# Kernel tuning notes

Hardware: AMD Instinct MI355X
Metric: run time of the kernel (lower is better)

## Reference

```python
import jax, jax.numpy as jnp
import numpy as np

B, S, D = 2, 2048, 1024
H = 16
HD = D // H  # 64
SCALE = HD ** -0.5


def setup_inputs() -> dict:
    key = jax.random.key(0)
    ks = jax.random.split(key, 9)
    init = lambda k, shape: jax.random.normal(k, shape, dtype=jnp.float32) * (1.0 / np.sqrt(shape[-1]))
    return {
        "x": jax.random.normal(ks[0], (B, S, D), dtype=jnp.float32),
        "wq": init(ks[1], (D, D)), "bq": jnp.zeros((D,), jnp.float32),
        "wk": init(ks[2], (D, D)), "bk": jnp.zeros((D,), jnp.float32),
        "wv": init(ks[3], (D, D)), "bv": jnp.zeros((D,), jnp.float32),
        "wo": init(ks[4], (D, D)), "bo": jnp.zeros((D,), jnp.float32),
    }


def reference(x, wq, bq, wk, bk, wv, bv, wo, bo):
    b, s, d = x.shape
    # projections -> [b, h, s, hd]
    q = (x @ wq + bq).reshape(b, s, H, HD).transpose(0, 2, 1, 3)
    k = (x @ wk + bk).reshape(b, s, H, HD).transpose(0, 2, 1, 3)
    v = (x @ wv + bv).reshape(b, s, H, HD).transpose(0, 2, 1, 3)
    # full causal attention (chunked loop in original computes exactly this)
    scores = jnp.einsum("bhqd,bhkd->bhqk", q, k) * SCALE
    causal = jnp.tril(jnp.ones((s, s), dtype=bool))
    scores = jnp.where(causal, scores, -jnp.inf)
    weights = jax.nn.softmax(scores, axis=-1)
    out = jnp.einsum("bhqk,bhkd->bhqd", weights, v)
    out = out.transpose(0, 2, 1, 3).reshape(b, s, d)
    return out @ wo + bo
```

## Files before the change

kernel.cpp:

```cpp
#include <hip/hip_runtime.h>
#include <hip/hip_bf16.h>
#include <cstdint>

#define B_  2
#define S_  2048
#define D_  1024
#define H_  16
#define HD_ 64
#define M_  (B_ * S_)
static constexpr float SC_LOG2E = 0.125f * 1.44269504088896f;

typedef __bf16 bf16x8 __attribute__((ext_vector_type(8)));
typedef __bf16 bf16x4 __attribute__((ext_vector_type(4)));
typedef float  f32x4  __attribute__((ext_vector_type(4)));

__device__ __forceinline__ unsigned short f2b(float f) {
  union { float f; unsigned u; } x; x.f = f;
  unsigned r = x.u + 0x7FFF + ((x.u >> 16) & 1);
  return (unsigned short)(r >> 16);
}

__device__ __forceinline__ void gl_lds16(const unsigned short* g, unsigned short* l) {
  __builtin_amdgcn_global_load_lds((const __attribute__((address_space(1))) void*)g,
                                   (__attribute__((address_space(3))) void*)l, 16, 0, 0);
}

__global__ void cvt_all_kernel(const float* __restrict__ x,
                               const float* __restrict__ w0, const float* __restrict__ w1,
                               const float* __restrict__ w2, const float* __restrict__ w3,
                               unsigned short* __restrict__ xb,
                               unsigned short* __restrict__ o0, unsigned short* __restrict__ o1,
                               unsigned short* __restrict__ o2, unsigned short* __restrict__ o3) {
  int tx = threadIdx.x, ty = threadIdx.y;
  if (blockIdx.z == 4) {
    int tid = ty * 32 + tx;
    int base = ((int)blockIdx.y * 32 + (int)blockIdx.x) * 1024 + tid;
    const float4* xf = (const float4*)x;
    ushort4* ob = (ushort4*)xb;
#pragma unroll
    for (int j = 0; j < 4; j++) {
      float4 v = xf[base + j * 256];
      ushort4 r;
      r.x = f2b(v.x); r.y = f2b(v.y); r.z = f2b(v.z); r.w = f2b(v.w);
      ob[base + j * 256] = r;
    }
    return;
  }
  const float* w = blockIdx.z == 0 ? w0 : blockIdx.z == 1 ? w1 : blockIdx.z == 2 ? w2 : w3;
  unsigned short* o = blockIdx.z == 0 ? o0 : blockIdx.z == 1 ? o1 : blockIdx.z == 2 ? o2 : o3;
  __shared__ float t[32][33];
  int x0 = blockIdx.x * 32, y0 = blockIdx.y * 32;
#pragma unroll
  for (int j = 0; j < 4; j++)
    t[ty + j * 8][tx] = w[(size_t)(y0 + ty + j * 8) * D_ + x0 + tx];
  __syncthreads();
#pragma unroll
  for (int j = 0; j < 4; j++)
    o[(size_t)(x0 + ty + j * 8) * D_ + y0 + tx] = f2b(t[tx][ty + j * 8]);
}

__global__ __launch_bounds__(256) void qkv_gemm_kernel(
    const unsigned short* __restrict__ xb,
    const unsigned short* __restrict__ wqt, const unsigned short* __restrict__ wkt,
    const unsigned short* __restrict__ wvt,
    const float* __restrict__ bq, const float* __restrict__ bk, const float* __restrict__ bv,
    unsigned short* __restrict__ qo, unsigned short* __restrict__ ko, unsigned short* __restrict__ vo) {
  const unsigned short* wt = blockIdx.z == 0 ? wqt : blockIdx.z == 1 ? wkt : wvt;
  const float* bias        = blockIdx.z == 0 ? bq  : blockIdx.z == 1 ? bk  : bv;
  unsigned short* out      = blockIdx.z == 0 ? qo  : blockIdx.z == 1 ? ko  : vo;
  const float scl = blockIdx.z == 0 ? SC_LOG2E : 1.0f;

  __shared__ __align__(16) unsigned short smem[4 * 128 * 32];
  unsigned short* pan[4] = { smem, smem + 4096, smem + 8192, smem + 12288 };
  const int tid = threadIdx.x;
  const int lane = tid & 63, wid = tid >> 6;
  const int wm = wid & 1, wn = wid >> 1;
  const int m0 = blockIdx.x * 128, n0 = blockIdx.y * 128;
  const int l15 = lane & 15, q4 = lane >> 4;

  f32x4 zero = {0.f, 0.f, 0.f, 0.f};
  f32x4 acc[4][4];
#pragma unroll
  for (int mt = 0; mt < 4; mt++)
#pragma unroll
    for (int nt = 0; nt < 4; nt++) acc[mt][nt] = zero;

  for (int kk = 0; kk < D_; kk += 64) {
#pragma unroll
    for (int i = 0; i < 2; i++) {
      int ci = tid + i * 256;
      int row = ci >> 2, kc = ci & 3;
      gl_lds16(xb + (size_t)(m0 + row) * D_ + kk      + kc * 8, pan[0] + ci * 8);
      gl_lds16(xb + (size_t)(m0 + row) * D_ + kk + 32 + kc * 8, pan[1] + ci * 8);
      gl_lds16(wt + (size_t)(n0 + row) * D_ + kk      + kc * 8, pan[2] + ci * 8);
      gl_lds16(wt + (size_t)(n0 + row) * D_ + kk + 32 + kc * 8, pan[3] + ci * 8);
    }
    __syncthreads();
#pragma unroll
    for (int kh = 0; kh < 2; kh++) {
      bf16x8 af[4], bfv[4];
#pragma unroll
      for (int mt = 0; mt < 4; mt++) af[mt]  = *(const bf16x8*)(pan[kh]     + (wm * 64 + mt * 16 + l15) * 32 + q4 * 8);
#pragma unroll
      for (int nt = 0; nt < 4; nt++) bfv[nt] = *(const bf16x8*)(pan[2 + kh] + (wn * 64 + nt * 16 + l15) * 32 + q4 * 8);
#pragma unroll
      for (int mt = 0; mt < 4; mt++)
#pragma unroll
        for (int nt = 0; nt < 4; nt++)
          acc[mt][nt] = __builtin_amdgcn_mfma_f32_16x16x32_bf16(af[mt], bfv[nt], acc[mt][nt], 0, 0, 0);
    }
    __syncthreads();
  }

  if (blockIdx.z < 2) {
#pragma unroll
    for (int nt = 0; nt < 4; nt++) {
      int n = n0 + wn * 64 + nt * 16 + l15;
      float bn = bias[n];
      int h = n >> 6, hd = n & 63;
#pragma unroll
      for (int mt = 0; mt < 4; mt++) {
#pragma unroll
        for (int r = 0; r < 4; r++) {
          int m = m0 + wm * 64 + mt * 16 + q4 * 4 + r;
          int b = m >> 11, s = m & (S_ - 1);
          out[(((size_t)(b * H_ + h)) * S_ + s) * HD_ + hd] = f2b((acc[mt][nt][r] + bn) * scl);
        }
      }
    }
  } else {
    unsigned short* buf = smem;
#pragma unroll
    for (int p = 0; p < 2; p++) {
      __syncthreads();
      if (wn == p) {
#pragma unroll
        for (int nt = 0; nt < 4; nt++) {
          int np = nt * 16 + l15;
          float bn = bias[n0 + p * 64 + np];
#pragma unroll
          for (int mt = 0; mt < 4; mt++) {
            f32x4 vb = acc[mt][nt];
            vb[0] += bn; vb[1] += bn; vb[2] += bn; vb[3] += bn;
            bf16x4 pk = __builtin_convertvector(vb, bf16x4);
            *(bf16x4*)(&buf[np * 136 + wm * 64 + mt * 16 + q4 * 4]) = pk;
          }
        }
      }
      __syncthreads();
#pragma unroll
      for (int i = 0; i < 4; i++) {
        int ci = tid + i * 256;
        int np = ci >> 4, c = ci & 15;
        int n = n0 + p * 64 + np;
        int h = n >> 6, hd = n & 63;
        int m = m0 + c * 8;
        int b = m >> 11, s = m & (S_ - 1);
        *(uint4*)(out + (((size_t)(b * H_ + h)) * HD_ + hd) * S_ + s) = *(const uint4*)(buf + np * 136 + c * 8);
      }
    }
  }
}

__global__ __launch_bounds__(512) void attn_kernel(
    const unsigned short* __restrict__ Q, const unsigned short* __restrict__ K,
    const unsigned short* __restrict__ Vt_g, unsigned short* __restrict__ O) {
  const int bh = blockIdx.y, b = bh >> 4, h = bh & 15;
  const unsigned short* Qh = Q    + (size_t)bh * S_ * HD_;
  const unsigned short* Kh = K    + (size_t)bh * S_ * HD_;
  const unsigned short* Vh = Vt_g + (size_t)bh * HD_ * S_;

  __shared__ __align__(16) unsigned short Ks[2][128 * 72];
  __shared__ __align__(16) unsigned short Vt[2][64 * 136];
  __shared__ __align__(16) unsigned short Ps[8][16 * 136];

  const int tid = threadIdx.x, lane = tid & 63, w = tid >> 6;
  const int l15 = lane & 15, q4 = lane >> 4;
  f32x4 zero = {0.f, 0.f, 0.f, 0.f};

  const int krow0 = tid >> 3, kcol0 = (tid & 7) * 8;
  const int vrow0 = tid >> 4, vcol0 = (tid & 15) * 8;

  int tc = 0;
  for (int half = 0; half < 2; half++) {
    const int qi = half ? (15 - (int)blockIdx.x) : (int)blockIdx.x;
    const int q0 = qi * 128;

    const unsigned short* qp = Qh + (size_t)(q0 + w * 16 + l15) * HD_ + q4 * 8;
    bf16x8 bq0 = *(const bf16x8*)(qp);
    bf16x8 bq1 = *(const bf16x8*)(qp + 32);

    float m_i = -1e30f, l_i = 0.f;
    f32x4 o_acc[4];
#pragma unroll
    for (int t = 0; t < 4; t++) o_acc[t] = zero;
    const int qrow = q0 + w * 16 + l15;
    const int nkt = qi + 1;

    uint4 kp0 = *(const uint4*)(Kh + (size_t)krow0 * HD_ + kcol0);
    uint4 kp1 = *(const uint4*)(Kh + (size_t)(krow0 + 64) * HD_ + kcol0);
    uint4 vp0 = *(const uint4*)(Vh + (size_t)vrow0 * S_ + vcol0);
    uint4 vp1 = *(const uint4*)(Vh + (size_t)(vrow0 + 32) * S_ + vcol0);

    for (int kt = 0; kt < nkt; kt++, tc++) {
      const int k0 = kt * 128;
      const int bi = tc & 1;
      unsigned short* Kb = Ks[bi];
      unsigned short* Vb = Vt[bi];
      *(uint4*)(Kb + krow0 * 72 + kcol0) = kp0;
      *(uint4*)(Kb + (krow0 + 64) * 72 + kcol0) = kp1;
      *(uint4*)(Vb + vrow0 * 136 + vcol0) = vp0;
      *(uint4*)(Vb + (vrow0 + 32) * 136 + vcol0) = vp1;
      __syncthreads();
      if (kt + 1 < nkt) {
        int kn = k0 + 128;
        kp0 = *(const uint4*)(Kh + (size_t)(kn + krow0) * HD_ + kcol0);
        kp1 = *(const uint4*)(Kh + (size_t)(kn + krow0 + 64) * HD_ + kcol0);
        vp0 = *(const uint4*)(Vh + (size_t)vrow0 * S_ + kn + vcol0);
        vp1 = *(const uint4*)(Vh + (size_t)(vrow0 + 32) * S_ + kn + vcol0);
      }

      f32x4 sc[8];
#pragma unroll
      for (int nt = 0; nt < 8; nt++) sc[nt] = zero;
#pragma unroll
      for (int nt = 0; nt < 8; nt++) {
        bf16x8 ak0 = *(const bf16x8*)(Kb + (nt * 16 + l15) * 72 + q4 * 8);
        bf16x8 ak1 = *(const bf16x8*)(Kb + (nt * 16 + l15) * 72 + 32 + q4 * 8);
        sc[nt] = __builtin_amdgcn_mfma_f32_16x16x32_bf16(ak0, bq0, sc[nt], 0, 0, 0);
        sc[nt] = __builtin_amdgcn_mfma_f32_16x16x32_bf16(ak1, bq1, sc[nt], 0, 0, 0);
      }

      const bool needMask = (k0 + 127) > (q0 + w * 16);
      float mx = m_i;
      if (needMask) {
#pragma unroll
        for (int nt = 0; nt < 8; nt++)
#pragma unroll
          for (int r = 0; r < 4; r++) {
            int key = k0 + nt * 16 + q4 * 4 + r;
            float v = (key > qrow) ? -1e30f : sc[nt][r];
            sc[nt][r] = v;
            mx = fmaxf(mx, v);
          }
      } else {
#pragma unroll
        for (int nt = 0; nt < 8; nt++)
#pragma unroll
          for (int r = 0; r < 4; r++) mx = fmaxf(mx, sc[nt][r]);
      }
      mx = fmaxf(mx, __shfl_xor(mx, 16));
      mx = fmaxf(mx, __shfl_xor(mx, 32));
      float alpha = __builtin_amdgcn_exp2f(m_i - mx);
      m_i = mx;
      float rs = 0.f;
#pragma unroll
      for (int nt = 0; nt < 8; nt++)
#pragma unroll
        for (int r = 0; r < 4; r++) {
          float p = __builtin_amdgcn_exp2f(sc[nt][r] - mx);
          sc[nt][r] = p;
          rs += p;
        }
      rs += __shfl_xor(rs, 16);
      rs += __shfl_xor(rs, 32);
      l_i = l_i * alpha + rs;

#pragma unroll
      for (int r = 0; r < 4; r++) {
        float ar = __shfl(alpha, q4 * 4 + r);
        o_acc[0][r] *= ar; o_acc[1][r] *= ar; o_acc[2][r] *= ar; o_acc[3][r] *= ar;
      }

#pragma unroll
      for (int nt = 0; nt < 8; nt++) {
        bf16x4 pk = __builtin_convertvector(sc[nt], bf16x4);
        *(bf16x4*)(&Ps[w][l15 * 136 + nt * 16 + q4 * 4]) = pk;
      }
      __threadfence_block();

#pragma unroll
      for (int ks = 0; ks < 4; ks++) {
        bf16x8 ap = *(const bf16x8*)(&Ps[w][l15 * 136 + ks * 32 + q4 * 8]);
#pragma unroll
        for (int nt2 = 0; nt2 < 4; nt2++) {
          bf16x8 bv = *(const bf16x8*)(Vb + (nt2 * 16 + l15) * 136 + ks * 32 + q4 * 8);
          o_acc[nt2] = __builtin_amdgcn_mfma_f32_16x16x32_bf16(ap, bv, o_acc[nt2], 0, 0, 0);
        }
      }
    }

#pragma unroll
    for (int r = 0; r < 4; r++) {
      float lr = __shfl(l_i, q4 * 4 + r);
      float inv = 1.0f / lr;
      int s = q0 + w * 16 + q4 * 4 + r;
#pragma unroll
      for (int nt2 = 0; nt2 < 4; nt2++)
        O[((size_t)(b * S_ + s)) * D_ + h * HD_ + nt2 * 16 + l15] = f2b(o_acc[nt2][r] * inv);
    }
  }
}

__global__ __launch_bounds__(256) void out_gemm_kernel(
    const unsigned short* __restrict__ ab, const unsigned short* __restrict__ wot,
    const float* __restrict__ bo, float* __restrict__ out) {
  __shared__ __align__(16) unsigned short smem[4 * 128 * 32];
  unsigned short* pan[4] = { smem, smem + 4096, smem + 8192, smem + 12288 };
  const int tid = threadIdx.x;
  const int lane = tid & 63, wid = tid >> 6;
  const int wm = wid & 1, wn = wid >> 1;
  const int m0 = blockIdx.x * 128, n0 = blockIdx.y * 128;
  const int l15 = lane & 15, q4 = lane >> 4;

  f32x4 zero = {0.f, 0.f, 0.f, 0.f};
  f32x4 acc[4][4];
#pragma unroll
  for (int mt = 0; mt < 4; mt++)
#pragma unroll
    for (int nt = 0; nt < 4; nt++) acc[mt][nt] = zero;

  for (int kk = 0; kk < D_; kk += 64) {
#pragma unroll
    for (int i = 0; i < 2; i++) {
      int ci = tid + i * 256;
      int row = ci >> 2, kc = ci & 3;
      gl_lds16(ab  + (size_t)(m0 + row) * D_ + kk      + kc * 8, pan[0] + ci * 8);
      gl_lds16(ab  + (size_t)(m0 + row) * D_ + kk + 32 + kc * 8, pan[1] + ci * 8);
      gl_lds16(wot + (size_t)(n0 + row) * D_ + kk      + kc * 8, pan[2] + ci * 8);
      gl_lds16(wot + (size_t)(n0 + row) * D_ + kk + 32 + kc * 8, pan[3] + ci * 8);
    }
    __syncthreads();
#pragma unroll
    for (int kh = 0; kh < 2; kh++) {
      bf16x8 af[4], bfv[4];
#pragma unroll
      for (int mt = 0; mt < 4; mt++) af[mt]  = *(const bf16x8*)(pan[kh]     + (wm * 64 + mt * 16 + l15) * 32 + q4 * 8);
#pragma unroll
      for (int nt = 0; nt < 4; nt++) bfv[nt] = *(const bf16x8*)(pan[2 + kh] + (wn * 64 + nt * 16 + l15) * 32 + q4 * 8);
#pragma unroll
      for (int mt = 0; mt < 4; mt++)
#pragma unroll
        for (int nt = 0; nt < 4; nt++)
          acc[mt][nt] = __builtin_amdgcn_mfma_f32_16x16x32_bf16(af[mt], bfv[nt], acc[mt][nt], 0, 0, 0);
    }
    __syncthreads();
  }

#pragma unroll
  for (int nt = 0; nt < 4; nt++) {
    int n = n0 + wn * 64 + nt * 16 + l15;
    float bn = bo[n];
#pragma unroll
    for (int mt = 0; mt < 4; mt++) {
#pragma unroll
      for (int r = 0; r < 4; r++) {
        int m = m0 + wm * 64 + mt * 16 + q4 * 4 + r;
        out[(size_t)m * D_ + n] = acc[mt][nt][r] + bn;
      }
    }
  }
}

extern "C" void kernel_launch(void* const* d_in, const int* in_sizes, int n_in,
                              void* d_out, int out_size, void* d_ws, size_t ws_size,
                              hipStream_t stream) {
  const float* x  = (const float*)d_in[0];
  const float* wq = (const float*)d_in[1];
  const float* bq = (const float*)d_in[2];
  const float* wk = (const float*)d_in[3];
  const float* bk = (const float*)d_in[4];
  const float* wv = (const float*)d_in[5];
  const float* bv = (const float*)d_in[6];
  const float* wo = (const float*)d_in[7];
  const float* bo = (const float*)d_in[8];
  float* out = (float*)d_out;

  char* ws = (char*)d_ws;
  unsigned short* xb  = (unsigned short*)(ws);
  unsigned short* wqt = (unsigned short*)(ws + (8u  << 20));
  unsigned short* wkt = (unsigned short*)(ws + (10u << 20));
  unsigned short* wvt = (unsigned short*)(ws + (12u << 20));
  unsigned short* wot = (unsigned short*)(ws + (14u << 20));
  unsigned short* qb  = (unsigned short*)(ws + (16u << 20));
  unsigned short* kb  = (unsigned short*)(ws + (24u << 20));
  unsigned short* vtg = (unsigned short*)(ws + (32u << 20));
  unsigned short* ab  = xb;

  cvt_all_kernel<<<dim3(32, 32, 5), dim3(32, 8), 0, stream>>>(x, wq, wk, wv, wo, xb, wqt, wkt, wvt, wot);
  qkv_gemm_kernel<<<dim3(32, 8, 3), dim3(256), 0, stream>>>(xb, wqt, wkt, wvt, bq, bk, bv, qb, kb, vtg);
  attn_kernel<<<dim3(8, B_ * H_), dim3(512), 0, stream>>>(qb, kb, vtg, ab);
  out_gemm_kernel<<<dim3(32, 8), dim3(256), 0, stream>>>(ab, wot, bo, out);
}
```

Measured before the change: 216.9 us.

## Double-buffer LDS tiles in QKV and output projection GEMMs

Reworks the K loop of both projection GEMMs to use two LDS buffers of 32-wide K slices. The next slice is prefetched with global_load_lds while MFMAs run on the current one, and there is one barrier per step instead of two. This is meant to hide global-to-LDS latency, but it halves the work per barrier and doubles the iteration count. There is also a possible hazard: the async LDS writes may not be waited on before the barrier, depending on how the compiler inserts vmcnt waits.

After: 182.8 us. 1.19x faster.

```diff
diff --git a/kernel.cpp b/kernel.cpp
--- a/kernel.cpp
+++ b/kernel.cpp
@@ -71,7 +71,6 @@
   const float scl = blockIdx.z == 0 ? SC_LOG2E : 1.0f;
 
   __shared__ __align__(16) unsigned short smem[4 * 128 * 32];
-  unsigned short* pan[4] = { smem, smem + 4096, smem + 8192, smem + 12288 };
   const int tid = threadIdx.x;
   const int lane = tid & 63, wid = tid >> 6;
   const int wm = wid & 1, wn = wid >> 1;
@@ -85,31 +84,38 @@
 #pragma unroll
     for (int nt = 0; nt < 4; nt++) acc[mt][nt] = zero;
 
-  for (int kk = 0; kk < D_; kk += 64) {
-#pragma unroll
-    for (int i = 0; i < 2; i++) {
-      int ci = tid + i * 256;
-      int row = ci >> 2, kc = ci & 3;
-      gl_lds16(xb + (size_t)(m0 + row) * D_ + kk      + kc * 8, pan[0] + ci * 8);
-      gl_lds16(xb + (size_t)(m0 + row) * D_ + kk + 32 + kc * 8, pan[1] + ci * 8);
-      gl_lds16(wt + (size_t)(n0 + row) * D_ + kk      + kc * 8, pan[2] + ci * 8);
-      gl_lds16(wt + (size_t)(n0 + row) * D_ + kk + 32 + kc * 8, pan[3] + ci * 8);
-    }
+#pragma unroll
+  for (int i = 0; i < 2; i++) {
+    int ci = tid + i * 256, row = ci >> 2, kc = ci & 3;
+    gl_lds16(xb + (size_t)(m0 + row) * D_ + kc * 8, smem + ci * 8);
+    gl_lds16(wt + (size_t)(n0 + row) * D_ + kc * 8, smem + 8192 + ci * 8);
+  }
+
+  int ib = 0;
+  for (int kk = 0; kk < D_; kk += 32, ib ^= 1) {
+    unsigned short* Ab = smem + ib * 4096;
+    unsigned short* Bb = smem + 8192 + ib * 4096;
+    unsigned short* An = smem + (ib ^ 1) * 4096;
+    unsigned short* Bn = smem + 8192 + (ib ^ 1) * 4096;
     __syncthreads();
-#pragma unroll
-    for (int kh = 0; kh < 2; kh++) {
-      bf16x8 af[4], bfv[4];
-#pragma unroll
-      for (int mt = 0; mt < 4; mt++) af[mt]  = *(const bf16x8*)(pan[kh]     + (wm * 64 + mt * 16 + l15) * 32 + q4 * 8);
-#pragma unroll
-      for (int nt = 0; nt < 4; nt++) bfv[nt] = *(const bf16x8*)(pan[2 + kh] + (wn * 64 + nt * 16 + l15) * 32 + q4 * 8);
-#pragma unroll
-      for (int mt = 0; mt < 4; mt++)
-#pragma unroll
-        for (int nt = 0; nt < 4; nt++)
-          acc[mt][nt] = __builtin_amdgcn_mfma_f32_16x16x32_bf16(af[mt], bfv[nt], acc[mt][nt], 0, 0, 0);
-    }
-    __syncthreads();
+    if (kk + 32 < D_) {
+#pragma unroll
+      for (int i = 0; i < 2; i++) {
+        int ci = tid + i * 256, row = ci >> 2, kc = ci & 3;
+        gl_lds16(xb + (size_t)(m0 + row) * D_ + kk + 32 + kc * 8, An + ci * 8);
+        gl_lds16(wt + (size_t)(n0 + row) * D_ + kk + 32 + kc * 8, Bn + ci * 8);
+      }
+    }
+    bf16x8 af[4], bfv[4];
+#pragma unroll
+    for (int mt = 0; mt < 4; mt++) af[mt]  = *(const bf16x8*)(Ab + (wm * 64 + mt * 16 + l15) * 32 + q4 * 8);
+#pragma unroll
+    for (int nt = 0; nt < 4; nt++) bfv[nt] = *(const bf16x8*)(Bb + (wn * 64 + nt * 16 + l15) * 32 + q4 * 8);
+#pragma unroll
+    for (int mt = 0; mt < 4; mt++)
+#pragma unroll
+      for (int nt = 0; nt < 4; nt++)
+        acc[mt][nt] = __builtin_amdgcn_mfma_f32_16x16x32_bf16(af[mt], bfv[nt], acc[mt][nt], 0, 0, 0);
   }
 
   if (blockIdx.z < 2) {
@@ -306,7 +312,6 @@
     const unsigned short* __restrict__ ab, const unsigned short* __restrict__ wot,
     const float* __restrict__ bo, float* __restrict__ out) {
   __shared__ __align__(16) unsigned short smem[4 * 128 * 32];
-  unsigned short* pan[4] = { smem, smem + 4096, smem + 8192, smem + 12288 };
   const int tid = threadIdx.x;
   const int lane = tid & 63, wid = tid >> 6;
   const int wm = wid & 1, wn = wid >> 1;
@@ -320,31 +325,38 @@
 #pragma unroll
     for (int nt = 0; nt < 4; nt++) acc[mt][nt] = zero;
 
-  for (int kk = 0; kk < D_; kk += 64) {
-#pragma unroll
-    for (int i = 0; i < 2; i++) {
-      int ci = tid + i * 256;
-      int row = ci >> 2, kc = ci & 3;
-      gl_lds16(ab  + (size_t)(m0 + row) * D_ + kk      + kc * 8, pan[0] + ci * 8);
-      gl_lds16(ab  + (size_t)(m0 + row) * D_ + kk + 32 + kc * 8, pan[1] + ci * 8);
-      gl_lds16(wot + (size_t)(n0 + row) * D_ + kk      + kc * 8, pan[2] + ci * 8);
-      gl_lds16(wot + (size_t)(n0 + row) * D_ + kk + 32 + kc * 8, pan[3] + ci * 8);
-    }
+#pragma unroll
+  for (int i = 0; i < 2; i++) {
+    int ci = tid + i * 256, row = ci >> 2, kc = ci & 3;
+    gl_lds16(ab  + (size_t)(m0 + row) * D_ + kc * 8, smem + ci * 8);
+    gl_lds16(wot + (size_t)(n0 + row) * D_ + kc * 8, smem + 8192 + ci * 8);
+  }
+
+  int ib = 0;
+  for (int kk = 0; kk < D_; kk += 32, ib ^= 1) {
+    unsigned short* Ab = smem + ib * 4096;
+    unsigned short* Bb = smem + 8192 + ib * 4096;
+    unsigned short* An = smem + (ib ^ 1) * 4096;
+    unsigned short* Bn = smem + 8192 + (ib ^ 1) * 4096;
     __syncthreads();
-#pragma unroll
-    for (int kh = 0; kh < 2; kh++) {
-      bf16x8 af[4], bfv[4];
-#pragma unroll
-      for (int mt = 0; mt < 4; mt++) af[mt]  = *(const bf16x8*)(pan[kh]     + (wm * 64 + mt * 16 + l15) * 32 + q4 * 8);
-#pragma unroll
-      for (int nt = 0; nt < 4; nt++) bfv[nt] = *(const bf16x8*)(pan[2 + kh] + (wn * 64 + nt * 16 + l15) * 32 + q4 * 8);
-#pragma unroll
-      for (int mt = 0; mt < 4; mt++)
-#pragma unroll
-        for (int nt = 0; nt < 4; nt++)
-          acc[mt][nt] = __builtin_amdgcn_mfma_f32_16x16x32_bf16(af[mt], bfv[nt], acc[mt][nt], 0, 0, 0);
-    }
-    __syncthreads();
+    if (kk + 32 < D_) {
+#pragma unroll
+      for (int i = 0; i < 2; i++) {
+        int ci = tid + i * 256, row = ci >> 2, kc = ci & 3;
+        gl_lds16(ab  + (size_t)(m0 + row) * D_ + kk + 32 + kc * 8, An + ci * 8);
+        gl_lds16(wot + (size_t)(n0 + row) * D_ + kk + 32 + kc * 8, Bn + ci * 8);
+      }
+    }
+    bf16x8 af[4], bfv[4];
+#pragma unroll
+    for (int mt = 0; mt < 4; mt++) af[mt]  = *(const bf16x8*)(Ab + (wm * 64 + mt * 16 + l15) * 32 + q4 * 8);
+#pragma unroll
+    for (int nt = 0; nt < 4; nt++) bfv[nt] = *(const bf16x8*)(Bb + (wn * 64 + nt * 16 + l15) * 32 + q4 * 8);
+#pragma unroll
+    for (int mt = 0; mt < 4; mt++)
+#pragma unroll
+      for (int nt = 0; nt < 4; nt++)
+        acc[mt][nt] = __builtin_amdgcn_mfma_f32_16x16x32_bf16(af[mt], bfv[nt], acc[mt][nt], 0, 0, 0);
   }
 
 #pragma unroll
```
